# Performance work log

Hardware: AMD Instinct MI355X
Metric: run time of the kernel (lower is better)

The kernel has to match this reference:

```python
import jax, jax.numpy as jnp
import numpy as np

W, E, D, NL, NC = 2048, 256, 512, 4, 5
DI, DS, DR, DC = 1024, 64, 32, 4  # d_inner=2*D, d_state, dt_rank=ceil(D/16), d_conv


def setup_inputs() -> dict:
    key = jax.random.key(0)
    ks = jax.random.split(key, 24)
    s = 0.02
    byte_sequence = jax.random.randint(ks[0], (2, W), 0, 256, dtype=jnp.int32)
    p = {
        "byte_sequence": byte_sequence,
        "byte_embed": jax.random.normal(ks[1], (256, E)) * s,
        "pos_embed": jax.random.normal(ks[2], (W, E)) * s,
        "in_w": jax.random.normal(ks[3], (D, E)) * s,
        "in_b": jnp.zeros((D,)),
        "ln_g": jnp.ones((NL, D)),
        "ln_b": jnp.zeros((NL, D)),
        "m_in_w": jax.random.normal(ks[4], (NL, 2 * DI, D)) * s,
        "conv_w": jax.random.normal(ks[5], (NL, DI, DC)) * s,
        "conv_b": jnp.zeros((NL, DI)),
        "xp_w": jax.random.normal(ks[6], (NL, DR + 2 * DS, DI)) * s,
        "dt_w": jax.random.normal(ks[7], (NL, DI, DR)) * s,
        "dt_b": jnp.full((NL, DI), -4.6),  # softplus(-4.6) ~ 0.01, in [dt_min, dt_max]
        "A_log": jnp.broadcast_to(jnp.log(jnp.arange(1.0, DS + 1.0)), (NL, DI, DS)) + 0.0,
        "Dp": jnp.ones((NL, DI)),
        "m_out_w": jax.random.normal(ks[8], (NL, D, DI)) * s,
        "h1_w": jax.random.normal(ks[9], (256, D)) * s,
        "h1_b": jnp.zeros((256,)),
        "h2_w": jax.random.normal(ks[10], (128, 256)) * s,
        "h2_b": jnp.zeros((128,)),
        "h3_w": jax.random.normal(ks[11], (NC, 128)) * s,
        "h3_b": jnp.zeros((NC,)),
    }
    return p


def _layernorm(x, g, b, eps=1e-5):
    mu = jnp.mean(x, axis=-1, keepdims=True)
    var = jnp.mean((x - mu) ** 2, axis=-1, keepdims=True)
    return (x - mu) * jax.lax.rsqrt(var + eps) * g + b


def _mamba(x, in_w, cw, cb, xp_w, dt_w, dt_b, A_log, Dp_, out_w):
    B, L, _ = x.shape
    xr = x @ in_w.T                       # [B,L,2*DI]
    xs, res = xr[..., :DI], xr[..., DI:]
    # causal depthwise conv1d over L
    xc = jnp.transpose(xs, (0, 2, 1))     # [B,DI,L]
    xc = jax.lax.conv_general_dilated(xc, cw[:, None, :], (1,), [(DC - 1, 0)], feature_group_count=DI)
    xs = jax.nn.silu(jnp.transpose(xc + cb[None, :, None], (0, 2, 1)))  # [B,L,DI]
    xdbl = xs @ xp_w.T                    # [B,L,DR+2*DS]
    dt, Bm, Cm = xdbl[..., :DR], xdbl[..., DR:DR + DS], xdbl[..., DR + DS:]
    delta = jax.nn.softplus(dt @ dt_w.T + dt_b)  # [B,L,DI]
    A = -jnp.exp(A_log)                   # [DI,DS]

    def step(h, inp):
        d_t, B_t, C_t, x_t = inp          # [B,DI],[B,DS],[B,DS],[B,DI]
        dA = jnp.exp(d_t[:, :, None] * A)             # [B,DI,DS]
        h = dA * h + (d_t * x_t)[:, :, None] * B_t[:, None, :]
        y = jnp.einsum('bds,bs->bd', h, C_t)
        return h, y

    h0 = jnp.zeros((B, DI, DS), x.dtype)
    seq = (jnp.swapaxes(delta, 0, 1), jnp.swapaxes(Bm, 0, 1), jnp.swapaxes(Cm, 0, 1), jnp.swapaxes(xs, 0, 1))
    _, ys = jax.lax.scan(step, h0, seq)   # ys: [L,B,DI]
    y = jnp.swapaxes(ys, 0, 1) + xs * Dp_
    y = y * jax.nn.silu(res)
    return y @ out_w.T


def reference(byte_sequence, byte_embed, pos_embed, in_w, in_b, ln_g, ln_b, m_in_w, conv_w, conv_b, xp_w, dt_w, dt_b, A_log, Dp, m_out_w, h1_w, h1_b, h2_w, h2_b, h3_w, h3_b):
    B, L = byte_sequence.shape
    x = byte_embed[byte_sequence] + pos_embed[None, :L]  # [B,L,E]
    x = x @ in_w.T + in_b                                # [B,L,D]
    for i in range(NL):
        res = x
        h = _layernorm(x, ln_g[i], ln_b[i])
        h = _mamba(h, m_in_w[i], conv_w[i], conv_b[i], xp_w[i], dt_w[i], dt_b[i], A_log[i], Dp[i], m_out_w[i])
        x = h + res
    h = jax.nn.relu(x @ h1_w.T + h1_b)
    h = jax.nn.relu(h @ h2_w.T + h2_b)
    return h @ h3_w.T + h3_b
```

## Files before the change

### kernel.cpp

```cpp
#include <hip/hip_runtime.h>
#include <hip/hip_bf16.h>

#define WLEN 2048
#define EDIM 256
#define DDIM 512
#define NLAYER 4
#define NCLS 5
#define DI 1024
#define DS 64
#define DR 32
#define DC 4
#define BB 2
#define TOK (BB*WLEN)
#define XD (DR + 2*DS)
#define CL 128
#define NCH (WLEN/CL)
#define LOG2E 1.44269504f

typedef __bf16 bf16x8 __attribute__((ext_vector_type(8)));
typedef float  f32x4  __attribute__((ext_vector_type(4)));

static __device__ __forceinline__ unsigned short f2bf(float f) {
    union { float f; unsigned u; } v; v.f = f;
    unsigned r = v.u + 0x7fffu + ((v.u >> 16) & 1u);
    return (unsigned short)(r >> 16);
}

__global__ __launch_bounds__(256) void embed_k(const int* __restrict__ seq,
    const float* __restrict__ be, const float* __restrict__ pe,
    float* __restrict__ out)
{
    int idx = blockIdx.x * 256 + threadIdx.x;
    int e  = idx & (EDIM - 1);
    int bl = idx >> 8;
    int l  = bl & (WLEN - 1);
    int tok = seq[bl];
    out[idx] = be[tok * EDIM + e] + pe[l * EDIM + e];
}

__global__ __launch_bounds__(256) void ln_k(const float* __restrict__ x,
    const float* __restrict__ g, const float* __restrict__ b,
    unsigned short* __restrict__ out)
{
    int row  = blockIdx.x * 4 + (threadIdx.x >> 6);
    int lane = threadIdx.x & 63;
    const float* xp = x + (size_t)row * DDIM;
    float v[8];
    float s = 0.f;
#pragma unroll
    for (int i = 0; i < 8; i++) { v[i] = xp[lane + 64 * i]; s += v[i]; }
#pragma unroll
    for (int off = 32; off; off >>= 1) s += __shfl_xor(s, off, 64);
    float mu = s * (1.f / 512.f);
    float s2 = 0.f;
#pragma unroll
    for (int i = 0; i < 8; i++) { float d = v[i] - mu; s2 += d * d; }
#pragma unroll
    for (int off = 32; off; off >>= 1) s2 += __shfl_xor(s2, off, 64);
    float rs = rsqrtf(s2 * (1.f / 512.f) + 1e-5f);
#pragma unroll
    for (int i = 0; i < 8; i++) {
        int c = lane + 64 * i;
        out[(size_t)row * DDIM + c] = f2bf((v[i] - mu) * rs * g[c] + b[c]);
    }
}

__global__ __launch_bounds__(256) void conv_t_k(const float* __restrict__ xcT,
    const float* __restrict__ cw, const float* __restrict__ cb,
    float* __restrict__ xsT)
{
    int gid  = blockIdx.x * 256 + threadIdx.x;
    int row  = gid >> 9;
    int col0 = (gid & 511) << 3;
    int l0   = col0 & (WLEN - 1);
    const float* src = xcT + (size_t)row * TOK + col0;
    float xw[12];
    if (l0 > 0) {
        float4 a = *(const float4*)(src - 4);
        xw[0] = a.x; xw[1] = a.y; xw[2] = a.z; xw[3] = a.w;
    } else {
        xw[0] = xw[1] = xw[2] = xw[3] = 0.f;
    }
    float4 m0 = *(const float4*)src;
    float4 m1 = *(const float4*)(src + 4);
    xw[4] = m0.x; xw[5] = m0.y; xw[6] = m0.z; xw[7] = m0.w;
    xw[8] = m1.x; xw[9] = m1.y; xw[10] = m1.z; xw[11] = m1.w;
    float w0 = cw[row * DC + 0], w1 = cw[row * DC + 1];
    float w2 = cw[row * DC + 2], w3 = cw[row * DC + 3];
    float bias = cb[row];
    float o[8];
#pragma unroll
    for (int u = 0; u < 8; u++) {
        float a = bias;
        a = fmaf(w0, xw[u + 1], a);
        a = fmaf(w1, xw[u + 2], a);
        a = fmaf(w2, xw[u + 3], a);
        a = fmaf(w3, xw[u + 4], a);
        o[u] = a / (1.f + __expf(-a));
    }
    float* dst = xsT + (size_t)row * TOK + col0;
    *(float4*)dst       = make_float4(o[0], o[1], o[2], o[3]);
    *(float4*)(dst + 4) = make_float4(o[4], o[5], o[6], o[7]);
}

__global__ __launch_bounds__(256) void f2bf_k(const float* __restrict__ in,
    unsigned short* __restrict__ out, int n)
{
    int i = blockIdx.x * 256 + threadIdx.x;
    if (i < n) out[i] = f2bf(in[i]);
}

__global__ __launch_bounds__(256) void trans_BC_k(const float* __restrict__ xdblT,
    float* __restrict__ BC)
{
    __shared__ float tile[64][65];
    int bt = blockIdx.x;
    int half = blockIdx.y;
    int col = threadIdx.x & 63, rr = threadIdx.x >> 6;
    int srow0 = DR + half * DS;
#pragma unroll
    for (int k = 0; k < 16; k++) {
        int i = k * 4 + rr;
        tile[i][col] = xdblT[(size_t)(srow0 + i) * TOK + bt * 64 + col];
    }
    __syncthreads();
#pragma unroll
    for (int k = 0; k < 16; k++) {
        int tt = k * 4 + rr;
        BC[(size_t)(bt * 64 + tt) * 128 + half * 64 + col] = tile[col][tt];
    }
}

__global__ __launch_bounds__(256) void trans_y_k(const float* __restrict__ yT,
    unsigned short* __restrict__ ybf)
{
    __shared__ float tile[64][65];
    int bt = blockIdx.x, bd = blockIdx.y, b = blockIdx.z;
    int col = threadIdx.x & 63, rr = threadIdx.x >> 6;
#pragma unroll
    for (int k = 0; k < 16; k++) {
        int i = k * 4 + rr;
        tile[i][col] = yT[(size_t)(bd * 64 + i) * TOK + b * WLEN + bt * 64 + col];
    }
    __syncthreads();
#pragma unroll
    for (int k = 0; k < 16; k++) {
        int tt = k * 4 + rr;
        ybf[((size_t)(b * WLEN + bt * 64 + tt)) * DI + bd * 64 + col] = f2bf(tile[col][tt]);
    }
}

#define SU 8

#define LOADG1(T0, dlt, xv, Bt, Ct)                                      \
  {                                                                      \
    *(float4*)&dlt[0] = *(const float4*)&dRow[(T0)];                     \
    *(float4*)&dlt[4] = *(const float4*)&dRow[(T0) + 4];                 \
    *(float4*)&xv[0]  = *(const float4*)&xRow[(T0)];                     \
    *(float4*)&xv[4]  = *(const float4*)&xRow[(T0) + 4];                 \
    const float* bc = BCrow + (size_t)(T0) * 128 + lane;                 \
    _Pragma("unroll")                                                    \
    for (int u = 0; u < SU; u++) {                                       \
      Bt[u] = bc[u * 128];                                               \
      Ct[u] = bc[u * 128 + 64];                                          \
    }                                                                    \
  }

#define COMPG1(T0, dlt, xv, Bt, Ct)                                      \
  {                                                                      \
    float dA[SU], p[SU], cds[SU];                                        \
    _Pragma("unroll")                                                    \
    for (int u = 0; u < SU; u++) dA[u] = __expf(dlt[u] * Aa);            \
    _Pragma("unroll")                                                    \
    for (int u = 0; u < SU; u++) {                                       \
      hst = fmaf(dA[u], hst, dlt[u] * xv[u] * Bt[u]);                    \
      p[u] = fmaf(xv[u], Dp0, hst * Ct[u]);                              \
    }                                                                    \
    cds[0] = cd + dlt[0];                                                \
    _Pragma("unroll")                                                    \
    for (int u = 1; u < SU; u++) cds[u] = cds[u - 1] + dlt[u];           \
    cd = cds[SU - 1];                                                    \
    if (lane == 0) {                                                     \
      *(float4*)&cdRow[(T0)]     = make_float4(cds[0], cds[1], cds[2], cds[3]); \
      *(float4*)&cdRow[(T0) + 4] = make_float4(cds[4], cds[5], cds[6], cds[7]); \
    }                                                                    \
    _Pragma("unroll")                                                    \
    for (int u = 0; u < SU; u++) wred[u * 64 + lane] = p[u];             \
    float4 q0 = *(const float4*)&wred[(lane >> 3) * 64 + (lane & 7) * 8];     \
    float4 q1 = *(const float4*)&wred[(lane >> 3) * 64 + (lane & 7) * 8 + 4]; \
    float sred = ((q0.x + q0.y) + (q0.z + q0.w)) +                       \
                 ((q1.x + q1.y) + (q1.z + q1.w));                        \
    sred += __shfl_xor(sred, 1, 64);                                     \
    sred += __shfl_xor(sred, 2, 64);                                     \
    sred += __shfl_xor(sred, 4, 64);                                     \
    if ((lane & 7) == 0) zRow[(T0) + (lane >> 3)] = sred;                \
  }

__global__ __launch_bounds__(256) void scan1_k(
    const float* __restrict__ deltaT,
    const float* __restrict__ BC,
    const float* __restrict__ xsT,
    const float* __restrict__ A_log,
    const float* __restrict__ Dp,
    float* __restrict__ zT,
    float* __restrict__ cdT,
    float* __restrict__ Hbuf,
    float* __restrict__ Sbuf)
{
    __shared__ float red[4 * SU * 64];
    int wv   = threadIdx.x >> 6;
    float* wred = red + wv * (SU * 64);
    int wid  = blockIdx.x * 4 + wv;
    int lane = threadIdx.x & 63;
    int c  = wid & (NCH - 1);
    int bd = wid >> 4;
    int d  = bd & (DI - 1);
    int b  = bd >> 10;
    size_t col0 = (size_t)b * WLEN + (size_t)c * CL;
    const float* dRow  = deltaT + (size_t)d * TOK + col0;
    const float* xRow  = xsT    + (size_t)d * TOK + col0;
    const float* BCrow = BC + col0 * 128;
    float* zRow  = zT  + (size_t)d * TOK + col0;
    float* cdRow = cdT + (size_t)d * TOK + col0;
    float Aa  = -__expf(A_log[d * DS + lane]);
    float Dp0 = (lane == 0) ? Dp[d] : 0.f;
    float hst = 0.f, cd = 0.f;

    float da[SU], xa[SU], Ba[SU], Ca[SU];
    float db[SU], xb[SU], Bb[SU], Cb[SU];

    LOADG1(0, da, xa, Ba, Ca)
    for (int t0 = 0; t0 < CL; t0 += 2 * SU) {
        LOADG1(t0 + SU, db, xb, Bb, Cb)
        COMPG1(t0, da, xa, Ba, Ca)
        if (t0 + 2 * SU < CL)
            LOADG1(t0 + 2 * SU, da, xa, Ba, Ca)
        COMPG1(t0 + SU, db, xb, Bb, Cb)
    }
    Hbuf[(size_t)wid * DS + lane] = hst;
    if (lane == 0) Sbuf[wid] = cd;
}

__global__ __launch_bounds__(256) void scan2_k(
    const float* __restrict__ Hbuf, const float* __restrict__ Sbuf,
    const float* __restrict__ A_log, float* __restrict__ h0buf)
{
    int bd   = blockIdx.x * 4 + (threadIdx.x >> 6);
    int lane = threadIdx.x & 63;
    int d = bd & (DI - 1);
    float Aa = -__expf(A_log[d * DS + lane]);
    float h = 0.f;
#pragma unroll
    for (int c = 0; c < NCH; c++) {
        size_t i = (size_t)bd * NCH + c;
        h0buf[i * DS + lane] = h;
        h = __expf(Aa * Sbuf[i]) * h + Hbuf[i * DS + lane];
    }
}

static __device__ __forceinline__ float lanef(float v, int s) {
    return __uint_as_float(__builtin_amdgcn_readlane(__float_as_uint(v), s));
}

__global__ __launch_bounds__(256) void scan3_k(
    const float* __restrict__ zT,
    const float* __restrict__ cdT,
    const float* __restrict__ rT,
    const float* __restrict__ xdblT,
    const float* __restrict__ A_log,
    const float* __restrict__ h0buf,
    float* __restrict__ yT)
{
    int wid  = blockIdx.x * 4 + (threadIdx.x >> 6);
    int lane = threadIdx.x & 63;
    int c  = wid & (NCH - 1);
    int bd = wid >> 4;
    int d  = bd & (DI - 1);
    int b  = bd >> 10;
    float Kv  = -__expf(A_log[d * DS + lane]) * LOG2E;
    float h0v = h0buf[(size_t)wid * DS + lane];
    size_t rowb = (size_t)d * TOK + (size_t)b * WLEN;
    const float* Cb = xdblT + (size_t)(DR + DS) * TOK + (size_t)b * WLEN;

#pragma unroll
    for (int pass = 0; pass < CL / 64; pass++) {
        int t = c * CL + pass * 64 + lane;
        float cd = cdT[rowb + t];
        float z  = zT[rowb + t];
        float r  = rT[rowb + t];
        float c0 = 0.f, c1 = 0.f, c2 = 0.f, c3 = 0.f;
#pragma unroll
        for (int s = 0; s < DS; s += 4) {
            float C0 = Cb[(size_t)(s + 0) * TOK + t];
            float C1 = Cb[(size_t)(s + 1) * TOK + t];
            float C2 = Cb[(size_t)(s + 2) * TOK + t];
            float C3 = Cb[(size_t)(s + 3) * TOK + t];
            c0 = fmaf(C0 * lanef(h0v, s + 0), exp2f(lanef(Kv, s + 0) * cd), c0);
            c1 = fmaf(C1 * lanef(h0v, s + 1), exp2f(lanef(Kv, s + 1) * cd), c1);
            c2 = fmaf(C2 * lanef(h0v, s + 2), exp2f(lanef(Kv, s + 2) * cd), c2);
            c3 = fmaf(C3 * lanef(h0v, s + 3), exp2f(lanef(Kv, s + 3) * cd), c3);
        }
        float corr = (c0 + c1) + (c2 + c3);
        float yv = (z + corr) * (r / (1.f + __expf(-r)));
        yT[rowb + t] = yv;
    }
}

template<int EPI>
__global__ __launch_bounds__(256) void gemm_bf16(
    const unsigned short* __restrict__ A,
    const unsigned short* __restrict__ W,
    const float* __restrict__ resid,
    float* __restrict__ C,
    float* __restrict__ T0buf,
    float* __restrict__ T1buf,
    int M, int N, int K)
{
    __shared__ unsigned short As[4 * 128 * 8];
    __shared__ unsigned short Bs[4 * 128 * 8];
    const int tid = threadIdx.x;
    const int bm = blockIdx.x * 128, bn = blockIdx.y * 128;
    const int l = tid & 63, w = tid >> 6;
    const int wm = (w >> 1) * 64, wn = (w & 1) * 64;
    const int srow = tid >> 1, shalf = tid & 1;
    const int kq = l >> 4, lr = l & 15;

    f32x4 acc[4][4];
#pragma unroll
    for (int i = 0; i < 4; i++)
#pragma unroll
        for (int j = 0; j < 4; j++)
            acc[i][j] = f32x4{0.f, 0.f, 0.f, 0.f};

    for (int k0 = 0; k0 < K; k0 += 32) {
        const uint4* ga = (const uint4*)(A + (size_t)(bm + srow) * K + k0 + shalf * 16);
        uint4 a0 = ga[0], a1 = ga[1];
        const uint4* gb = (const uint4*)(W + (size_t)(bn + srow) * K + k0 + shalf * 16);
        uint4 b0 = gb[0], b1 = gb[1];
        __syncthreads();
        int kg = shalf * 2;
        *(uint4*)&As[((kg    ) * 128 + srow) * 8] = a0;
        *(uint4*)&As[((kg + 1) * 128 + srow) * 8] = a1;
        *(uint4*)&Bs[((kg    ) * 128 + srow) * 8] = b0;
        *(uint4*)&Bs[((kg + 1) * 128 + srow) * 8] = b1;
        __syncthreads();
        bf16x8 av[4], bv[4];
#pragma unroll
        for (int mf = 0; mf < 4; mf++)
            av[mf] = *(const bf16x8*)&As[(kq * 128 + wm + mf * 16 + lr) * 8];
#pragma unroll
        for (int nf = 0; nf < 4; nf++)
            bv[nf] = *(const bf16x8*)&Bs[(kq * 128 + wn + nf * 16 + lr) * 8];
#pragma unroll
        for (int mf = 0; mf < 4; mf++)
#pragma unroll
            for (int nf = 0; nf < 4; nf++)
                acc[mf][nf] = __builtin_amdgcn_mfma_f32_16x16x32_bf16(
                    av[mf], bv[nf], acc[mf][nf], 0, 0, 0);
    }
#pragma unroll
    for (int mf = 0; mf < 4; mf++) {
#pragma unroll
        for (int nf = 0; nf < 4; nf++) {
            int n  = bn + wn + nf * 16 + lr;
            int m0 = bm + wm + mf * 16 + kq * 4;
            if (EPI == 5) {
                float4 val = make_float4(acc[mf][nf][0], acc[mf][nf][1],
                                         acc[mf][nf][2], acc[mf][nf][3]);
                float* dst = (n < DI) ? &T0buf[(size_t)n * TOK + m0]
                                      : &T1buf[(size_t)(n - DI) * TOK + m0];
                *(float4*)dst = val;
            } else {
#pragma unroll
                for (int r = 0; r < 4; r++) {
                    int m = m0 + r;
                    float v = acc[mf][nf][r];
                    if (EPI == 4) v += resid[(size_t)m * N + n];
                    C[(size_t)m * N + n] = v;
                }
            }
        }
    }
}

template<int EPI>
__global__ __launch_bounds__(256) void gemm_nn(
    const float* __restrict__ A,
    const float* __restrict__ B,
    const float* __restrict__ bias,
    float* __restrict__ C,
    int M, int N, int K)
{
    __shared__ float As[16][64];
    __shared__ float Bs[16][64];
    const int tid = threadIdx.x;
    const int tx = tid & 15, ty = tid >> 4;
    const int bm = blockIdx.x * 64, bn = blockIdx.y * 64;
    const int arow = tid >> 2, ak = (tid & 3) << 2;
    const int brow = tid & 15, bn4 = (tid >> 4) << 2;
    float acc[4][4] = {};
    for (int k0 = 0; k0 < K; k0 += 16) {
        float4 av = make_float4(0.f, 0.f, 0.f, 0.f);
        if (bm + arow < M)
            av = *(const float4*)&A[(size_t)(bm + arow) * K + k0 + ak];
        float4 bv = *(const float4*)&B[(size_t)(k0 + brow) * N + bn + bn4];
        __syncthreads();
        As[ak + 0][arow] = av.x; As[ak + 1][arow] = av.y;
        As[ak + 2][arow] = av.z; As[ak + 3][arow] = av.w;
        *(float4*)&Bs[brow][bn4] = bv;
        __syncthreads();
#pragma unroll
        for (int k = 0; k < 16; ++k) {
            float4 a = *(const float4*)&As[k][ty * 4];
            float4 w = *(const float4*)&Bs[k][tx * 4];
            float aa[4] = {a.x, a.y, a.z, a.w};
            float ww[4] = {w.x, w.y, w.z, w.w};
#pragma unroll
            for (int i = 0; i < 4; i++)
#pragma unroll
                for (int j = 0; j < 4; j++)
                    acc[i][j] = fmaf(aa[i], ww[j], acc[i][j]);
        }
        __syncthreads();
    }
#pragma unroll
    for (int i = 0; i < 4; i++) {
        int m = bm + ty * 4 + i;
        if (m >= M) continue;
        float vv[4];
#pragma unroll
        for (int j = 0; j < 4; j++) {
            float v = acc[i][j];
            if (EPI == 3) {
                v += bias[m];
                v = fmaxf(v, 0.f) + log1pf(__expf(-fabsf(v)));
            }
            vv[j] = v;
        }
        *(float4*)&C[(size_t)m * N + bn + tx * 4] = make_float4(vv[0], vv[1], vv[2], vv[3]);
    }
}

template<int EPI>
__global__ __launch_bounds__(256) void gemm_nt(
    const float* __restrict__ A, int lda,
    const float* __restrict__ W, int ldw,
    const float* __restrict__ bias,
    float* __restrict__ C, int ldc,
    int M, int N, int K)
{
    __shared__ float As[16][64];
    __shared__ float Ws[16][64];
    const int tid = threadIdx.x;
    const int tx = tid & 15;
    const int ty = tid >> 4;
    const int bm = blockIdx.x * 64;
    const int bn = blockIdx.y * 64;
    const int lr = tid >> 2;
    const int lc = (tid & 3) << 2;
    float acc[4][4] = {};
    for (int k0 = 0; k0 < K; k0 += 16) {
        float4 av = *(const float4*)(A + (size_t)(bm + lr) * lda + (k0 + lc));
        float4 wv = make_float4(0.f, 0.f, 0.f, 0.f);
        if (bn + lr < N)
            wv = *(const float4*)(W + (size_t)(bn + lr) * ldw + (k0 + lc));
        As[lc + 0][lr] = av.x; As[lc + 1][lr] = av.y;
        As[lc + 2][lr] = av.z; As[lc + 3][lr] = av.w;
        Ws[lc + 0][lr] = wv.x; Ws[lc + 1][lr] = wv.y;
        Ws[lc + 2][lr] = wv.z; Ws[lc + 3][lr] = wv.w;
        __syncthreads();
#pragma unroll
        for (int k = 0; k < 16; ++k) {
            float4 a = *(const float4*)&As[k][ty * 4];
            float4 w = *(const float4*)&Ws[k][tx * 4];
            float aa[4] = {a.x, a.y, a.z, a.w};
            float ww[4] = {w.x, w.y, w.z, w.w};
#pragma unroll
            for (int i = 0; i < 4; i++)
#pragma unroll
                for (int j = 0; j < 4; j++)
                    acc[i][j] = fmaf(aa[i], ww[j], acc[i][j]);
        }
        __syncthreads();
    }
#pragma unroll
    for (int i = 0; i < 4; i++) {
        int m = bm + ty * 4 + i;
#pragma unroll
        for (int j = 0; j < 4; j++) {
            int n = bn + tx * 4 + j;
            if (n >= N) continue;
            float v = acc[i][j];
            v += bias[n];
            if (EPI == 2) v = fmaxf(v, 0.f);
            C[(size_t)m * ldc + n] = v;
        }
    }
}

extern "C" void kernel_launch(void* const* d_in, const int* in_sizes, int n_in,
                              void* d_out, int out_size, void* d_ws, size_t ws_size,
                              hipStream_t stream)
{
    const int*   seq        = (const int*)d_in[0];
    const float* byte_embed = (const float*)d_in[1];
    const float* pos_embed  = (const float*)d_in[2];
    const float* in_w       = (const float*)d_in[3];
    const float* in_b       = (const float*)d_in[4];
    const float* ln_g       = (const float*)d_in[5];
    const float* ln_b       = (const float*)d_in[6];
    const float* m_in_w     = (const float*)d_in[7];
    const float* conv_w     = (const float*)d_in[8];
    const float* conv_b     = (const float*)d_in[9];
    const float* xp_w       = (const float*)d_in[10];
    const float* dt_w       = (const float*)d_in[11];
    const float* dt_b       = (const float*)d_in[12];
    const float* A_log      = (const float*)d_in[13];
    const float* Dp         = (const float*)d_in[14];
    const float* m_out_w    = (const float*)d_in[15];
    const float* h1_w       = (const float*)d_in[16];
    const float* h1_b       = (const float*)d_in[17];
    const float* h2_w       = (const float*)d_in[18];
    const float* h2_b       = (const float*)d_in[19];
    const float* h3_w       = (const float*)d_in[20];
    const float* h3_b       = (const float*)d_in[21];
    float* out = (float*)d_out;

    float* ws = (float*)d_ws;
    size_t off = 0;
    float* xe     = ws + off; off += (size_t)TOK * EDIM;
    float* x      = ws + off; off += (size_t)TOK * DDIM;
    float* xcT    = ws + off; off += (size_t)DI * TOK;
    float* xsT    = ws + off; off += (size_t)DI * TOK;
    float* xdblT  = ws + off; off += (size_t)XD * TOK;
    float* BC     = ws + off; off += (size_t)TOK * 2 * DS;
    float* deltaT = ws + off; off += (size_t)DI * TOK;
    float* zT     = ws + off; off += (size_t)DI * TOK;
    float* cdT    = ws + off; off += (size_t)DI * TOK;
    float* rT     = ws + off; off += (size_t)DI * TOK;
    float* Hbuf   = ws + off; off += (size_t)BB * DI * NCH * DS;
    float* h0buf  = ws + off; off += (size_t)BB * DI * NCH * DS;
    float* Sbuf   = ws + off; off += (size_t)BB * DI * NCH;
    unsigned short* h_bf   = (unsigned short*)(ws + off); off += (size_t)TOK * DDIM / 2;
    unsigned short* y_bf   = (unsigned short*)(ws + off); off += (size_t)TOK * DI / 2;
    unsigned short* wmi_bf = (unsigned short*)(ws + off); off += (size_t)NLAYER * 2 * DI * DDIM / 2;
    unsigned short* wmo_bf = (unsigned short*)(ws + off); off += (size_t)NLAYER * DDIM * DI / 2;
    float* yT = deltaT;
    float* t1 = xe;
    float* t2 = (float*)h_bf;

    {
        int n1 = NLAYER * 2 * DI * DDIM;
        f2bf_k<<<(n1 + 255) / 256, 256, 0, stream>>>(m_in_w, wmi_bf, n1);
        int n2 = NLAYER * DDIM * DI;
        f2bf_k<<<(n2 + 255) / 256, 256, 0, stream>>>(m_out_w, wmo_bf, n2);
    }

    embed_k<<<TOK * EDIM / 256, 256, 0, stream>>>(seq, byte_embed, pos_embed, xe);
    gemm_nt<1><<<dim3(TOK/64, DDIM/64), 256, 0, stream>>>(
        xe, EDIM, in_w, EDIM, in_b, x, DDIM, TOK, DDIM, EDIM);

    for (int i = 0; i < NLAYER; i++) {
        const float* lg  = ln_g  + (size_t)i * DDIM;
        const float* lb  = ln_b  + (size_t)i * DDIM;
        const unsigned short* miw = wmi_bf + (size_t)i * 2 * DI * DDIM;
        const float* cw  = conv_w + (size_t)i * DI * DC;
        const float* cb  = conv_b + (size_t)i * DI;
        const float* xpw = xp_w  + (size_t)i * XD * DI;
        const float* dtw = dt_w  + (size_t)i * DI * DR;
        const float* dtb = dt_b  + (size_t)i * DI;
        const float* al  = A_log + (size_t)i * DI * DS;
        const float* dp  = Dp    + (size_t)i * DI;
        const unsigned short* mow = wmo_bf + (size_t)i * DDIM * DI;

        ln_k<<<TOK/4, 256, 0, stream>>>(x, lg, lb, h_bf);
        gemm_bf16<5><<<dim3(TOK/128, 2*DI/128), 256, 0, stream>>>(
            h_bf, miw, nullptr, nullptr, xcT, rT, TOK, 2*DI, DDIM);
        conv_t_k<<<(DI * TOK / 8) / 256, 256, 0, stream>>>(xcT, cw, cb, xsT);
        gemm_nn<0><<<dim3((XD + 63) / 64, TOK / 64), 256, 0, stream>>>(
            xpw, xsT, nullptr, xdblT, XD, TOK, DI);
        trans_BC_k<<<dim3(TOK/64, 2), 256, 0, stream>>>(xdblT, BC);
        gemm_nn<3><<<dim3(DI / 64, TOK / 64), 256, 0, stream>>>(
            dtw, xdblT, dtb, deltaT, DI, TOK, DR);

        scan1_k<<<(BB*DI*NCH)/4, 256, 0, stream>>>(
            deltaT, BC, xsT, al, dp, zT, cdT, Hbuf, Sbuf);
        scan2_k<<<(BB*DI)/4, 256, 0, stream>>>(Hbuf, Sbuf, al, h0buf);
        scan3_k<<<(BB*DI*NCH)/4, 256, 0, stream>>>(
            zT, cdT, rT, xdblT, al, h0buf, yT);
        trans_y_k<<<dim3(WLEN/64, DI/64, BB), 256, 0, stream>>>(yT, y_bf);

        gemm_bf16<4><<<dim3(TOK/128, DDIM/128), 256, 0, stream>>>(
            y_bf, mow, x, x, nullptr, nullptr, TOK, DDIM, DI);
    }

    gemm_nt<2><<<dim3(TOK/64, 256/64), 256, 0, stream>>>(
        x, DDIM, h1_w, DDIM, h1_b, t1, 256, TOK, 256, DDIM);
    gemm_nt<2><<<dim3(TOK/64, 2), 256, 0, stream>>>(
        t1, 256, h2_w, 256, h2_b, t2, 128, TOK, 128, 256);
    gemm_nt<1><<<dim3(TOK/64, 1), 256, 0, stream>>>(
        t2, 128, h3_w, 128, h3_b, out, NCLS, TOK, NCLS, 128);
}
```

Measured before the change: 1.916 ms.

## Interleave B/C layout and software-pipeline scan recurrence with LDS reduction

```diff
diff --git a/kernel.cpp b/kernel.cpp
--- a/kernel.cpp
+++ b/kernel.cpp
@@ -127,7 +127,7 @@
 #pragma unroll
     for (int k = 0; k < 16; k++) {
         int tt = k * 4 + rr;
-        BC[(size_t)(bt * 64 + tt) * 128 + half * 64 + col] = tile[col][tt];
+        BC[(size_t)(bt * 64 + tt) * 128 + col * 2 + half] = tile[col][tt];
     }
 }
 
@@ -158,23 +158,23 @@
     *(float4*)&dlt[4] = *(const float4*)&dRow[(T0) + 4];                 \
     *(float4*)&xv[0]  = *(const float4*)&xRow[(T0)];                     \
     *(float4*)&xv[4]  = *(const float4*)&xRow[(T0) + 4];                 \
-    const float* bc = BCrow + (size_t)(T0) * 128 + lane;                 \
+    const float2* bc = (const float2*)(BCrow + (size_t)(T0) * 128) + lane; \
     _Pragma("unroll")                                                    \
     for (int u = 0; u < SU; u++) {                                       \
-      Bt[u] = bc[u * 128];                                               \
-      Ct[u] = bc[u * 128 + 64];                                          \
+      float2 v2 = bc[u * 64];                                            \
+      Bt[u] = v2.x; Ct[u] = v2.y;                                        \
     }                                                                    \
   }
 
-#define COMPG1(T0, dlt, xv, Bt, Ct)                                      \
+#define RECUR(T0, dlt, xv, Bt, Ct, WRED)                                 \
   {                                                                      \
-    float dA[SU], p[SU], cds[SU];                                        \
+    float dA[SU], cds[SU];                                               \
     _Pragma("unroll")                                                    \
     for (int u = 0; u < SU; u++) dA[u] = __expf(dlt[u] * Aa);            \
     _Pragma("unroll")                                                    \
     for (int u = 0; u < SU; u++) {                                       \
       hst = fmaf(dA[u], hst, dlt[u] * xv[u] * Bt[u]);                    \
-      p[u] = fmaf(xv[u], Dp0, hst * Ct[u]);                              \
+      WRED[u * 64 + lane] = fmaf(xv[u], Dp0, hst * Ct[u]);               \
     }                                                                    \
     cds[0] = cd + dlt[0];                                                \
     _Pragma("unroll")                                                    \
@@ -184,10 +184,12 @@
       *(float4*)&cdRow[(T0)]     = make_float4(cds[0], cds[1], cds[2], cds[3]); \
       *(float4*)&cdRow[(T0) + 4] = make_float4(cds[4], cds[5], cds[6], cds[7]); \
     }                                                                    \
-    _Pragma("unroll")                                                    \
-    for (int u = 0; u < SU; u++) wred[u * 64 + lane] = p[u];             \
-    float4 q0 = *(const float4*)&wred[(lane >> 3) * 64 + (lane & 7) * 8];     \
-    float4 q1 = *(const float4*)&wred[(lane >> 3) * 64 + (lane & 7) * 8 + 4]; \
+  }
+
+#define REDUCE(T0, WRED)                                                 \
+  {                                                                      \
+    float4 q0 = *(const float4*)&WRED[(lane >> 3) * 64 + (lane & 7) * 8];     \
+    float4 q1 = *(const float4*)&WRED[(lane >> 3) * 64 + (lane & 7) * 8 + 4]; \
     float sred = ((q0.x + q0.y) + (q0.z + q0.w)) +                       \
                  ((q1.x + q1.y) + (q1.z + q1.w));                        \
     sred += __shfl_xor(sred, 1, 64);                                     \
@@ -207,9 +209,10 @@
     float* __restrict__ Hbuf,
     float* __restrict__ Sbuf)
 {
-    __shared__ float red[4 * SU * 64];
+    __shared__ float red[4 * 2 * SU * 64];
     int wv   = threadIdx.x >> 6;
-    float* wred = red + wv * (SU * 64);
+    float* w0 = red + wv * (2 * SU * 64);
+    float* w1 = w0 + SU * 64;
     int wid  = blockIdx.x * 4 + wv;
     int lane = threadIdx.x & 63;
     int c  = wid & (NCH - 1);
@@ -230,12 +233,15 @@
     float db[SU], xb[SU], Bb[SU], Cb[SU];
 
     LOADG1(0, da, xa, Ba, Ca)
+    LOADG1(SU, db, xb, Bb, Cb)
+    RECUR(0, da, xa, Ba, Ca, w0)
     for (int t0 = 0; t0 < CL; t0 += 2 * SU) {
-        LOADG1(t0 + SU, db, xb, Bb, Cb)
-        COMPG1(t0, da, xa, Ba, Ca)
-        if (t0 + 2 * SU < CL)
-            LOADG1(t0 + 2 * SU, da, xa, Ba, Ca)
-        COMPG1(t0 + SU, db, xb, Bb, Cb)
+        if (t0 + 2 * SU < CL) LOADG1(t0 + 2 * SU, da, xa, Ba, Ca)
+        RECUR(t0 + SU, db, xb, Bb, Cb, w1)
+        REDUCE(t0, w0)
+        if (t0 + 3 * SU < CL) LOADG1(t0 + 3 * SU, db, xb, Bb, Cb)
+        if (t0 + 2 * SU < CL) RECUR(t0 + 2 * SU, da, xa, Ba, Ca, w0)
+        REDUCE(t0 + SU, w1)
     }
     Hbuf[(size_t)wid * DS + lane] = hst;
     if (lane == 0) Sbuf[wid] = cd;
```

Result: slower. 2.120 ms (+10.7%).
